# Performance work log

Measured on AMD Instinct MI355X. Metric: run time of the kernel, lower is better.

## Reference

```python
import jax, jax.numpy as jnp
import numpy as np

D, N, K, H, F, L, T, V = 2048, 16, 8, 128, 6144, 2, 2048, 32000
EPS = 1e-6
THETA = 1000000.0

def rms_norm(x, scale, eps=EPS):
    x32 = x.astype(jnp.float32)
    y = x32 * jax.lax.rsqrt(jnp.mean(x32 * x32, axis=-1, keepdims=True) + eps)
    return (y * scale).astype(x.dtype)

def apply_rope(x, pos, dim, theta):
    # x: [T, n, H]; rotate_half style RoPE on first `dim` dims (dim == H here)
    half = dim // 2
    inv_freq = 1.0 / (theta ** (jnp.arange(half, dtype=jnp.float32) / half))
    freqs = pos.astype(jnp.float32)[:, None] * inv_freq  # [T, half]
    cos = jnp.cos(freqs)[:, None, :]
    sin = jnp.sin(freqs)[:, None, :]
    x1, x2 = x[..., :half], x[..., half:]
    return jnp.concatenate([x1 * cos - x2 * sin, x2 * cos + x1 * sin], axis=-1).astype(x.dtype)

def qmatmul(x, w, s):
    # fp8 e4m3 dequant matmul: quantize kernel, upcast, scale per output channel
    wq = w.astype(jnp.float8_e4m3fn).astype(jnp.float32)
    return (x @ wq) * s

def setup_inputs() -> dict:
    key = jax.random.key(0)
    ks = jax.random.split(key, 20)
    w = lambda k, sh, sc=0.02: (jax.random.normal(k, sh, jnp.float32) * sc)
    return {
        'input_ids': jax.random.randint(ks[0], (T,), 0, V, jnp.int32),
        'positions': jnp.arange(T, dtype=jnp.int32),
        'embed': w(ks[1], (V, D), 1.0),
        'ln1': jax.random.uniform(ks[2], (L, D), jnp.float32),
        'q_w': w(ks[3], (L, D, N, H)),
        'q_norm': jax.random.uniform(ks[4], (L, H), jnp.float32),
        'k_w': w(ks[5], (L, D, K, H)),
        'k_norm': jax.random.uniform(ks[6], (L, H), jnp.float32),
        'v_w': w(ks[7], (L, D, K, H)),
        'o_w': w(ks[8], (L, N, H, D)),
        'ln2': jax.random.uniform(ks[9], (L, D), jnp.float32),
        'gate_w': w(ks[10], (L, D, F), 0.1),
        'gate_scale': jax.random.uniform(ks[11], (L, F), jnp.float32, 0.01, 0.05),
        'up_w': w(ks[12], (L, D, F), 0.1),
        'up_scale': jax.random.uniform(ks[13], (L, F), jnp.float32, 0.01, 0.05),
        'down_w': w(ks[14], (L, F, D), 0.1),
        'down_scale': jax.random.uniform(ks[15], (L, D), jnp.float32, 0.01, 0.05),
        'final_norm': jax.random.uniform(ks[16], (D,), jnp.float32),
        'lm_head': w(ks[17], (D, V), 0.02),
    }

def reference(input_ids, positions, embed, ln1, q_w, q_norm, k_w, k_norm, v_w, o_w,
              ln2, gate_w, gate_scale, up_w, up_scale, down_w, down_scale,
              final_norm, lm_head):
    h = embed[input_ids]                                   # [T, D]
    t = h.shape[0]
    sm_scale = 1.0 / np.sqrt(H)
    causal = jnp.tril(jnp.ones((t, t), dtype=bool))
    G = N // K  # GQA group size

    def layer(h, p):
        l1, qw, qn, kw, kn, vw, ow, l2, gw, gs, uw, us, dw, ds = p
        x = rms_norm(h, l1)
        q = rms_norm(jnp.einsum('td,dnh->tnh', x, qw), qn)
        q = apply_rope(q, positions, H, THETA)
        k = rms_norm(jnp.einsum('td,dkh->tkh', x, kw), kn)
        k = apply_rope(k, positions, H, THETA)
        v = jnp.einsum('td,dkh->tkh', x, vw)
        qg = q.reshape(t, K, G, H)
        scores = jnp.einsum('tkgh,skh->kgts', qg, k) * sm_scale
        scores = jnp.where(causal[None, None], scores, -1e30)
        attn = jax.nn.softmax(scores, axis=-1)
        o = jnp.einsum('kgts,skh->tkgh', attn, v).reshape(t, N, H)
        h = h + jnp.einsum('tnh,nhd->td', o, ow)
        x2 = rms_norm(h, l2)
        fuse = jax.nn.silu(qmatmul(x2, gw, gs)) * qmatmul(x2, uw, us)
        h = h + qmatmul(fuse, dw, ds)
        return h, None

    h, _ = jax.lax.scan(layer, h, (ln1, q_w, q_norm, k_w, k_norm, v_w, o_w,
                                   ln2, gate_w, gate_scale, up_w, up_scale,
                                   down_w, down_scale))
    h = rms_norm(h, final_norm)
    return h @ lm_head                                      # [T, V] logits
```

## Files before the change

### kernel.cpp

```cpp
#include <hip/hip_runtime.h>

#define TT 2048
#define DD 2048
#define NHEAD 16
#define KHEAD 8
#define HDIM 128
#define FF 6144
#define LLAYERS 2
#define VV 32000

typedef __attribute__((ext_vector_type(8))) __bf16 bf16x8;
typedef __attribute__((ext_vector_type(4))) float f32x4;

__device__ __forceinline__ unsigned short f2bf(float x) {
  unsigned u = __float_as_uint(x);
  return (unsigned short)((u + 0x7FFFu + ((u >> 16) & 1u)) >> 16);
}

__device__ __forceinline__ float fp8_rt(float x) {
  float ax = fabsf(x);
  if (ax < 0.015625f) return rintf(x * 512.0f) * (1.0f / 512.0f);
  unsigned u = __float_as_uint(x);
  unsigned r = (u + 0x7FFFFu + ((u >> 20) & 1u)) & 0xFFF00000u;
  float y = __uint_as_float(r);
  if (fabsf(y) > 448.0f) y = copysignf(448.0f, x);
  return y;
}

__device__ __forceinline__ void gload16(const void* g, void* l) {
  __builtin_amdgcn_global_load_lds((__attribute__((address_space(1))) void*)g,
                                   (__attribute__((address_space(3))) void*)l,
                                   16, 0, 0);
}

__global__ void k_embed(const int* __restrict__ ids, const float* __restrict__ embed,
                        float* __restrict__ h) {
  int t = blockIdx.x;
  const float4* src = (const float4*)(embed + (size_t)ids[t] * DD);
  float4* dst = (float4*)(h + (size_t)t * DD);
  for (int i = threadIdx.x; i < DD / 4; i += 256) dst[i] = src[i];
}

__global__ void k_rmsnorm(const float* __restrict__ h, const float* __restrict__ g,
                          unsigned short* __restrict__ out) {
  int t = blockIdx.x;
  const float4* row = (const float4*)(h + (size_t)t * DD);
  float4 a = row[threadIdx.x], b = row[threadIdx.x + 256];
  float ss = a.x * a.x + a.y * a.y + a.z * a.z + a.w * a.w +
             b.x * b.x + b.y * b.y + b.z * b.z + b.w * b.w;
#pragma unroll
  for (int m = 32; m >= 1; m >>= 1) ss += __shfl_xor(ss, m);
  __shared__ float sred[4];
  int wid = threadIdx.x >> 6;
  if ((threadIdx.x & 63) == 0) sred[wid] = ss;
  __syncthreads();
  float tot = sred[0] + sred[1] + sred[2] + sred[3];
  float rn = 1.0f / sqrtf(tot * (1.0f / 2048.0f) + 1e-6f);
  const float4* gg = (const float4*)g;
  float4 g0 = gg[threadIdx.x], g1 = gg[threadIdx.x + 256];
  unsigned short* o0 = out + (size_t)t * DD + threadIdx.x * 4;
  unsigned short* o1 = o0 + 1024;
  *(ushort4*)o0 = make_ushort4(f2bf(a.x * rn * g0.x), f2bf(a.y * rn * g0.y),
                               f2bf(a.z * rn * g0.z), f2bf(a.w * rn * g0.w));
  *(ushort4*)o1 = make_ushort4(f2bf(b.x * rn * g1.x), f2bf(b.y * rn * g1.y),
                               f2bf(b.z * rn * g1.z), f2bf(b.w * rn * g1.w));
}

template <bool QUANT>
__global__ void k_wconv(const float* __restrict__ W, unsigned short* __restrict__ Wt,
                        int Kd, int Nd) {
  __shared__ float tile[64][65];
  int k0 = blockIdx.y * 64, n0 = blockIdx.x * 64;
  int t = threadIdx.x;
#pragma unroll
  for (int i = 0; i < 4; ++i) {
    int row = (t >> 4) + i * 16, c4 = (t & 15) * 4;
    float4 v = *(const float4*)&W[(size_t)(k0 + row) * Nd + n0 + c4];
    tile[row][c4] = v.x; tile[row][c4 + 1] = v.y;
    tile[row][c4 + 2] = v.z; tile[row][c4 + 3] = v.w;
  }
  __syncthreads();
#pragma unroll
  for (int i = 0; i < 2; ++i) {
    int n = (t >> 3) + i * 32, kc = (t & 7) * 8;
    unsigned short r[8];
#pragma unroll
    for (int j = 0; j < 8; ++j) {
      float x = tile[kc + j][n];
      if (QUANT) x = fp8_rt(x);
      r[j] = f2bf(x);
    }
    unsigned short* o = &Wt[(size_t)(n0 + n) * Kd + k0 + kc];
    *(ushort4*)o = make_ushort4(r[0], r[1], r[2], r[3]);
    *(ushort4*)(o + 4) = make_ushort4(r[4], r[5], r[6], r[7]);
  }
}

template <int EPI>
__global__ __launch_bounds__(256, 2) void k_gemm(
    const unsigned short* __restrict__ A, const unsigned short* __restrict__ Bt,
    int M, int N, int K, float* __restrict__ Cf, const float* __restrict__ scaleN) {
  __shared__ unsigned short Al[128 * 64];
  __shared__ unsigned short Bl[128 * 64];
  const int tid = threadIdx.x;
  const int lane = tid & 63, wid = tid >> 6;
  const int wm = wid >> 1, wn = wid & 1;
  const int l16 = lane & 15, lg = lane >> 4;
  const size_t m0 = (size_t)blockIdx.x * 128, n0 = (size_t)blockIdx.y * 128;
  f32x4 acc[4][4] = {};
  for (int k0 = 0; k0 < K; k0 += 64) {
    __syncthreads();
#pragma unroll
    for (int it = 0; it < 4; ++it) {
      int chunk = it * 256 + tid;
      int row = chunk >> 3, c8 = chunk & 7;
      const unsigned short* ga = A + (m0 + row) * (size_t)K + k0 + c8 * 8;
      const unsigned short* gb = Bt + (n0 + row) * (size_t)K + k0 + c8 * 8;
      int base = (it * 256 + wid * 64) * 8;
      gload16((const void*)ga, (void*)&Al[base]);
      gload16((const void*)gb, (void*)&Bl[base]);
    }
    __syncthreads();
#pragma unroll
    for (int kk = 0; kk < 2; ++kk) {
      bf16x8 af[4], bfr[4];
      const int kb = kk * 32 + lg * 8;
#pragma unroll
      for (int i = 0; i < 4; ++i)
        af[i] = *(const bf16x8*)&Al[(wm * 64 + i * 16 + l16) * 64 + kb];
#pragma unroll
      for (int i = 0; i < 4; ++i)
        bfr[i] = *(const bf16x8*)&Bl[(wn * 64 + i * 16 + l16) * 64 + kb];
#pragma unroll
      for (int mi = 0; mi < 4; ++mi)
#pragma unroll
        for (int ni = 0; ni < 4; ++ni)
          acc[mi][ni] = __builtin_amdgcn_mfma_f32_16x16x32_bf16(af[mi], bfr[ni],
                                                                acc[mi][ni], 0, 0, 0);
    }
  }
#pragma unroll
  for (int mi = 0; mi < 4; ++mi)
#pragma unroll
    for (int r = 0; r < 4; ++r) {
      size_t row = m0 + wm * 64 + mi * 16 + 4 * lg + r;
#pragma unroll
      for (int ni = 0; ni < 4; ++ni) {
        size_t col = n0 + wn * 64 + ni * 16 + l16;
        float v = acc[mi][ni][r];
        size_t idx = row * (size_t)N + col;
        if constexpr (EPI == 0) Cf[idx] = v;
        else if constexpr (EPI == 1) Cf[idx] += v;
        else Cf[idx] += v * scaleN[col];
      }
    }
}

template <int PT, bool VM, class STG>
__device__ __forceinline__ void gphase(const char* smem, int BUF, int aRd, int bRd,
                                       bf16x8 (&af)[4][2], bf16x8 (&bfr)[2][2][2],
                                       f32x4 (&acc)[8][4], STG&& stage, bool vmzero) {
  constexpr int MH = (PT >= 2) ? 1 : 0;
  constexpr int NH = (PT == 1 || PT == 2) ? 1 : 0;
  if constexpr (PT == 0 || PT == 2) {
#pragma unroll
    for (int m = 0; m < 4; ++m) {
      int abase = BUF + aRd + MH * 8192 + m * 2048;
      af[m][0] = *(const bf16x8*)(smem + abase);
      af[m][1] = *(const bf16x8*)(smem + (abase ^ 64));
    }
  }
  if constexpr (PT <= 1) {
#pragma unroll
    for (int n = 0; n < 2; ++n) {
      int bbase = BUF + bRd + NH * 4096 + n * 2048;
      bfr[NH][n][0] = *(const bf16x8*)(smem + bbase);
      bfr[NH][n][1] = *(const bf16x8*)(smem + (bbase ^ 64));
    }
  }
  stage();
  if (VM) {
    if (vmzero) asm volatile("s_waitcnt vmcnt(0)" ::: "memory");
    else        asm volatile("s_waitcnt vmcnt(4)" ::: "memory");
  }
  __builtin_amdgcn_sched_barrier(0);
  __builtin_amdgcn_s_barrier();
  if constexpr (PT != 3) {
    asm volatile("s_waitcnt lgkmcnt(0)" ::: "memory");
    __builtin_amdgcn_sched_barrier(0);
  }
  __builtin_amdgcn_s_setprio(1);
#pragma unroll
  for (int kk = 0; kk < 2; ++kk)
#pragma unroll
    for (int m = 0; m < 4; ++m)
#pragma unroll
      for (int n = 0; n < 2; ++n)
        acc[MH * 4 + m][NH * 2 + n] = __builtin_amdgcn_mfma_f32_16x16x32_bf16(
            af[m][kk], bfr[NH][n][kk], acc[MH * 4 + m][NH * 2 + n], 0, 0, 0);
  __builtin_amdgcn_s_setprio(0);
  __builtin_amdgcn_sched_barrier(0);
}

template <int EPI>
__global__ __launch_bounds__(512, 2) void k_gemm256(
    const unsigned short* __restrict__ A, const unsigned short* __restrict__ Bt,
    int N, int Kstride, int Kloop, int S, void* __restrict__ Cv) {
  extern __shared__ __align__(16) char smem[];
  const int tid = threadIdx.x;
  const int lane = tid & 63, wid = tid >> 6;
  const int wm = wid >> 2, wn = wid & 3;
  const int l16 = lane & 15, lg = lane >> 4;
  const int l8 = lane >> 3, s8 = lane & 7;

  const int nwg = gridDim.x;
  const int q = nwg >> 3, r = nwg & 7;
  const int xcd = blockIdx.x & 7, loc = blockIdx.x >> 3;
  const int wg = (xcd < r ? xcd * (q + 1) : r * (q + 1) + (xcd - r) * q) + loc;
  const int bm = wg & 7;
  const int t_ = wg >> 3;
  const int split = t_ % S, bn = t_ / S;
  const size_t m0 = (size_t)bm * 256, n0 = (size_t)bn * 256;
  const size_t kofs = (size_t)split * Kloop;

  const char* Ag = (const char*)(A + m0 * (size_t)Kstride + kofs);
  const char* Bg = (const char*)(Bt + n0 * (size_t)Kstride + kofs);
  const size_t sKA = (size_t)Kstride * 128;
  const size_t sKB = (size_t)Kstride * 64;
  const size_t aA = (size_t)(wid * 8 + l8) * Kstride * 2 + (size_t)((s8 ^ l8) << 4);
  const size_t aB = (size_t)((wid & 3) * 8 + l8) * Kstride * 2 + (size_t)((s8 ^ l8) << 4);

  auto stgA = [&](int BUF, int p, int kt) {
    gload16(Ag + aA + (size_t)p * sKA + (size_t)kt * 128,
            smem + BUF + p * 8192 + wid * 1024);
  };
  auto stgB = [&](int BUF, int qa, int qb, int kt) {
    int qq = (wid < 4) ? qa : qb;
    gload16(Bg + aB + (size_t)qq * sKB + (size_t)kt * 128,
            smem + BUF + 32768 + qq * 4096 + (wid & 3) * 1024);
  };
  auto stAev = [&](int BUF, int kt) { stgA(BUF, 0, kt); stgA(BUF, 2, kt); };
  auto stAod = [&](int BUF, int kt) { stgA(BUF, 1, kt); stgA(BUF, 3, kt); };
  auto stBev = [&](int BUF, int kt) { stgB(BUF, 0, 2, kt); stgB(BUF, 4, 6, kt); };
  auto stBod = [&](int BUF, int kt) { stgB(BUF, 1, 3, kt); stgB(BUF, 5, 7, kt); };

  const int colx = (lg << 4) ^ ((l16 & 7) << 4);
  const int aRd = (wm * 128 + l16) * 128 + colx;
  const int bRd = 32768 + (wn * 64 + l16) * 128 + colx;

  f32x4 acc[8][4] = {};
  bf16x8 af[4][2];
  bf16x8 bfr[2][2][2];

  stAev(0, 0); stAod(0, 0); stBev(0, 0); stBod(0, 0);
  stBev(65536, 1); stBod(65536, 1);
  asm volatile("s_waitcnt vmcnt(4)" ::: "memory");
  __builtin_amdgcn_s_barrier();

  const int NIT = Kloop >> 7;
#pragma unroll 1
  for (int i = 0; i < NIT; ++i) {
    const int t1 = 2 * i + 1, t2 = 2 * i + 2, t3 = 2 * i + 3;
    const bool more = (i + 1 < NIT);
    gphase<0, false>(smem, 0, aRd, bRd, af, bfr, acc, [&] { stAev(65536, t1); }, false);
    gphase<1, false>(smem, 0, aRd, bRd, af, bfr, acc, [&] { stAod(65536, t1); }, false);
    gphase<2, false>(smem, 0, aRd, bRd, af, bfr, acc, [&] { if (more) stBev(0, t2); }, false);
    gphase<3, true >(smem, 0, aRd, bRd, af, bfr, acc, [&] { if (more) stBod(0, t2); }, !more);
    gphase<0, false>(smem, 65536, aRd, bRd, af, bfr, acc, [&] { if (more) stAev(0, t2); }, false);
    gphase<1, false>(smem, 65536, aRd, bRd, af, bfr, acc, [&] { if (more) stAod(0, t2); }, false);
    gphase<2, false>(smem, 65536, aRd, bRd, af, bfr, acc, [&] { if (more) stBev(65536, t3); }, false);
    gphase<3, true >(smem, 65536, aRd, bRd, af, bfr, acc, [&] { if (more) stBod(65536, t3); }, false);
  }

  char* Cb = (char*)Cv + (EPI == 0 ? (size_t)split * TT * N * 4 : 0);
#pragma unroll
  for (int m = 0; m < 8; ++m)
#pragma unroll
    for (int rr = 0; rr < 4; ++rr) {
      size_t row = m0 + wm * 128 + m * 16 + lg * 4 + rr;
#pragma unroll
      for (int n = 0; n < 4; ++n) {
        size_t col = n0 + wn * 64 + n * 16 + l16;
        float v = acc[m][n][rr];
        size_t idx = row * (size_t)N + col;
        if constexpr (EPI == 0) ((float*)Cb)[idx] = v;
        else ((unsigned short*)Cb)[idx] = f2bf(v);
      }
    }
}

__global__ void k_sred(const float* __restrict__ p, const float* __restrict__ scale,
                       float* __restrict__ h, int S, int n) {
  int total = TT * n / 4;
  for (int i = blockIdx.x * 256 + threadIdx.x; i < total; i += gridDim.x * 256) {
    float4 s = ((const float4*)p)[i];
    for (int ss = 1; ss < S; ++ss) {
      float4 v = ((const float4*)(p + (size_t)ss * TT * n))[i];
      s.x += v.x; s.y += v.y; s.z += v.z; s.w += v.w;
    }
    if (scale) {
      int col = (i * 4) % n;
      s.x *= scale[col]; s.y *= scale[col + 1];
      s.z *= scale[col + 2]; s.w *= scale[col + 3];
    }
    float4 hv = ((float4*)h)[i];
    hv.x += s.x; hv.y += s.y; hv.z += s.z; hv.w += s.w;
    ((float4*)h)[i] = hv;
  }
}

__global__ void k_swiglu(const unsigned short* __restrict__ gu, const float* __restrict__ gs,
                         const float* __restrict__ us, unsigned short* __restrict__ out) {
  size_t idx = (size_t)blockIdx.x * 256 + threadIdx.x;
  int t = idx / 768, f8 = (int)(idx % 768) * 8;
  const unsigned short* gp = gu + (size_t)t * 12288 + f8;
  ushort4 ga = *(const ushort4*)gp, gb = *(const ushort4*)(gp + 4);
  ushort4 ua = *(const ushort4*)(gp + 6144), ub = *(const ushort4*)(gp + 6148);
  unsigned short* op = out + (size_t)t * FF + f8;
  unsigned short res[8];
  unsigned short gv[8] = {ga.x, ga.y, ga.z, ga.w, gb.x, gb.y, gb.z, gb.w};
  unsigned short uv[8] = {ua.x, ua.y, ua.z, ua.w, ub.x, ub.y, ub.z, ub.w};
#pragma unroll
  for (int j = 0; j < 8; ++j) {
    float g = __uint_as_float((unsigned)gv[j] << 16) * gs[f8 + j];
    float u = __uint_as_float((unsigned)uv[j] << 16) * us[f8 + j];
    float f = (g / (1.0f + expf(-g))) * u;
    res[j] = f2bf(f);
  }
  *(ushort4*)op = make_ushort4(res[0], res[1], res[2], res[3]);
  *(ushort4*)(op + 4) = make_ushort4(res[4], res[5], res[6], res[7]);
}

__global__ void k_qk_post(const float* __restrict__ p0, const float* __restrict__ p1,
                          const float* __restrict__ nscale, const int* __restrict__ pos,
                          unsigned short* __restrict__ out, int nheads, int rstride,
                          int coloff, float qscale) {
  int gw = blockIdx.x * 4 + (threadIdx.x >> 6);
  int t = gw / nheads, n = gw % nheads;
  int lane = threadIdx.x & 63;
  size_t base = (size_t)t * rstride + coloff + n * HDIM;
  float x1 = p0[base + lane] + p1[base + lane];
  float x2 = p0[base + lane + 64] + p1[base + lane + 64];
  float ss = x1 * x1 + x2 * x2;
#pragma unroll
  for (int m = 32; m >= 1; m >>= 1) ss += __shfl_xor(ss, m);
  float rn = qscale / sqrtf(ss * (1.0f / 128.0f) + 1e-6f);
  x1 *= rn * nscale[lane];
  x2 *= rn * nscale[lane + 64];
  float p = (float)pos[t];
  float inv = powf(1.0e6f, -(float)lane / 64.0f);
  float fr = p * inv;
  float c = cosf(fr), s = sinf(fr);
  unsigned short* o = out + ((size_t)n * TT + t) * HDIM;
  o[lane] = f2bf(x1 * c - x2 * s);
  o[lane + 64] = f2bf(x2 * c + x1 * s);
}

__global__ void k_vt(const float* __restrict__ p0, const float* __restrict__ p1,
                     unsigned short* __restrict__ vT, int rstride) {
  __shared__ float tile[32][33];
  int t0 = blockIdx.x * 32, h0 = blockIdx.y * 32;
  int tx = threadIdx.x, ty = threadIdx.y;
#pragma unroll
  for (int i = 0; i < 32; i += 8) {
    size_t idx = (size_t)(t0 + ty + i) * rstride + h0 + tx;
    tile[ty + i][tx] = p0[idx] + p1[idx];
  }
  __syncthreads();
  int kvh = h0 >> 7;
  int hh = h0 & 127;
#pragma unroll
  for (int i = 0; i < 32; i += 8) {
    float x = tile[tx][ty + i];
    vT[(size_t)kvh * HDIM * TT + (size_t)(hh + ty + i) * TT + t0 + tx] = f2bf(x);
  }
}

__global__ __launch_bounds__(256, 2) void k_attn(
    const unsigned short* __restrict__ Qb, const unsigned short* __restrict__ Kb,
    const unsigned short* __restrict__ Vt, unsigned short* __restrict__ Ob) {
  __shared__ __align__(16) char kv[2][32768];
  __shared__ __align__(16) char Pl[4][2048];
  const int tid = threadIdx.x;
  const int w = tid >> 6, lane = tid & 63;
  const int l16 = lane & 15, lg = lane >> 4;
  const int head = blockIdx.y, kvh = head >> 1;
  const int r0 = blockIdx.x * 64 + w * 16;

  bf16x8 qf[4];
  const unsigned short* Qrow = Qb + ((size_t)head * TT + r0 + l16) * HDIM;
#pragma unroll
  for (int kc = 0; kc < 4; ++kc) qf[kc] = *(const bf16x8*)&Qrow[kc * 32 + lg * 8];

  const char* Kh = (const char*)(Kb + (size_t)kvh * TT * HDIM);
  const char* Vh = (const char*)(Vt + (size_t)kvh * HDIM * TT);

  auto stage = [&](int buf, int t) {
    const int kt0 = t * 64;
    char* bk = kv[buf];
    char* bv = kv[buf] + 16384;
#pragma unroll
    for (int it = 0; it < 4; ++it) {
      int rowK = it * 16 + w * 4 + (lane >> 4);
      gload16(Kh + (size_t)(kt0 + rowK) * 256 + (((lane & 15) ^ (rowK & 7)) << 4),
              bk + (it * 256 + w * 64) * 16);
      int rowV = it * 32 + w * 8 + (lane >> 3);
      gload16(Vh + (size_t)rowV * (TT * 2) + (size_t)kt0 * 2 +
                  (((lane & 7) ^ (rowV & 7)) << 4),
              bv + (it * 256 + w * 64) * 16);
    }
  };

  f32x4 o[8] = {};
  float m_[4], l_[4];
#pragma unroll
  for (int r = 0; r < 4; ++r) { m_[r] = -1e30f; l_[r] = 0.0f; }
  char* Pw = Pl[w];

  const int nt = blockIdx.x + 1;
  stage(0, 0);
  asm volatile("s_waitcnt vmcnt(0)" ::: "memory");
  __syncthreads();

#pragma unroll 1
  for (int t = 0; t < nt; ++t) {
    const int buf = t & 1;
    const int kt0 = t * 64;
    if (t + 1 < nt) stage(buf ^ 1, t + 1);
    const char* bk = kv[buf];
    const char* bv = kv[buf] + 16384;

    f32x4 sg[4];
#pragma unroll
    for (int g = 0; g < 4; ++g) {
      sg[g] = f32x4{0.f, 0.f, 0.f, 0.f};
#pragma unroll
      for (int kc = 0; kc < 4; ++kc) {
        int row = g * 16 + l16;
        int slot = kc * 4 + lg;
        bf16x8 kf = *(const bf16x8*)(bk + row * 256 + ((slot ^ (row & 7)) << 4));
        sg[g] = __builtin_amdgcn_mfma_f32_16x16x32_bf16(qf[kc], kf, sg[g], 0, 0, 0);
      }
    }
    f32x4 mx;
#pragma unroll
    for (int r = 0; r < 4; ++r) {
      int row = r0 + 4 * lg + r;
      float a = sg[0][r]; if (kt0 + l16 > row) a = -1e30f; sg[0][r] = a;
      float b = sg[1][r]; if (kt0 + 16 + l16 > row) b = -1e30f; sg[1][r] = b;
      float c = sg[2][r]; if (kt0 + 32 + l16 > row) c = -1e30f; sg[2][r] = c;
      float d = sg[3][r]; if (kt0 + 48 + l16 > row) d = -1e30f; sg[3][r] = d;
      mx[r] = fmaxf(fmaxf(a, b), fmaxf(c, d));
    }
#pragma unroll
    for (int msk = 8; msk >= 1; msk >>= 1)
#pragma unroll
      for (int r = 0; r < 4; ++r) mx[r] = fmaxf(mx[r], __shfl_xor(mx[r], msk));
    float alpha[4];
#pragma unroll
    for (int r = 0; r < 4; ++r) {
      float mn = fmaxf(m_[r], mx[r]);
      alpha[r] = __expf(m_[r] - mn);
      m_[r] = mn;
    }
    f32x4 rs;
#pragma unroll
    for (int r = 0; r < 4; ++r) {
      float s0 = __expf(sg[0][r] - m_[r]);
      float s1 = __expf(sg[1][r] - m_[r]);
      float s2 = __expf(sg[2][r] - m_[r]);
      float s3 = __expf(sg[3][r] - m_[r]);
      sg[0][r] = s0; sg[1][r] = s1; sg[2][r] = s2; sg[3][r] = s3;
      rs[r] = (s0 + s1) + (s2 + s3);
    }
#pragma unroll
    for (int msk = 8; msk >= 1; msk >>= 1)
#pragma unroll
      for (int r = 0; r < 4; ++r) rs[r] += __shfl_xor(rs[r], msk);
#pragma unroll
    for (int r = 0; r < 4; ++r) l_[r] = l_[r] * alpha[r] + rs[r];
#pragma unroll
    for (int hi = 0; hi < 8; ++hi)
#pragma unroll
      for (int r = 0; r < 4; ++r) o[hi][r] *= alpha[r];

#pragma unroll
    for (int g = 0; g < 4; ++g)
#pragma unroll
      for (int r = 0; r < 4; ++r) {
        int prow = 4 * lg + r;
        int slot = g * 2 + (l16 >> 3);
        *(unsigned short*)(Pw + prow * 128 + ((slot ^ (prow & 7)) << 4) +
                           (l16 & 7) * 2) = f2bf(sg[g][r]);
      }
    bf16x8 pf[2];
#pragma unroll
    for (int half = 0; half < 2; ++half) {
      int slot = half * 4 + lg;
      pf[half] = *(const bf16x8*)(Pw + l16 * 128 + ((slot ^ (l16 & 7)) << 4));
    }
#pragma unroll
    for (int hi = 0; hi < 8; ++hi) {
      int row = hi * 16 + l16;
#pragma unroll
      for (int half = 0; half < 2; ++half) {
        int slot = half * 4 + lg;
        bf16x8 vf = *(const bf16x8*)(bv + row * 128 + ((slot ^ (row & 7)) << 4));
        o[hi] = __builtin_amdgcn_mfma_f32_16x16x32_bf16(pf[half], vf, o[hi], 0, 0, 0);
      }
    }
    asm volatile("s_waitcnt vmcnt(0)" ::: "memory");
    __syncthreads();
  }

#pragma unroll
  for (int r = 0; r < 4; ++r) {
    float inv = 1.0f / l_[r];
    size_t t = r0 + 4 * lg + r;
#pragma unroll
    for (int hi = 0; hi < 8; ++hi)
      Ob[t * DD + head * HDIM + hi * 16 + l16] = f2bf(o[hi][r] * inv);
  }
}

extern "C" void kernel_launch(void* const* d_in, const int* in_sizes, int n_in,
                              void* d_out, int out_size, void* d_ws, size_t ws_size,
                              hipStream_t stream) {
  (void)in_sizes; (void)n_in; (void)out_size; (void)ws_size;
  const int* ids = (const int*)d_in[0];
  const int* pos = (const int*)d_in[1];
  const float* embed = (const float*)d_in[2];
  const float* ln1 = (const float*)d_in[3];
  const float* q_w = (const float*)d_in[4];
  const float* q_norm = (const float*)d_in[5];
  const float* k_w = (const float*)d_in[6];
  const float* k_norm = (const float*)d_in[7];
  const float* v_w = (const float*)d_in[8];
  const float* o_w = (const float*)d_in[9];
  const float* ln2 = (const float*)d_in[10];
  const float* gate_w = (const float*)d_in[11];
  const float* gate_s = (const float*)d_in[12];
  const float* up_w = (const float*)d_in[13];
  const float* up_s = (const float*)d_in[14];
  const float* down_w = (const float*)d_in[15];
  const float* down_s = (const float*)d_in[16];
  const float* fnorm = (const float*)d_in[17];
  const float* lm = (const float*)d_in[18];

  hipFuncSetAttribute((const void*)k_gemm256<0>,
                      hipFuncAttributeMaxDynamicSharedMemorySize, 131072);
  hipFuncSetAttribute((const void*)k_gemm256<1>,
                      hipFuncAttributeMaxDynamicSharedMemorySize, 131072);

  char* p = (char*)d_ws;
  auto alloc = [&](size_t n) { char* r = p; p += (n + 255) & ~(size_t)255; return r; };
  unsigned short* wbuf = (unsigned short*)alloc((size_t)VV * DD * 2);
  float* h = (float*)alloc((size_t)TT * DD * 4);
  unsigned short* xb = (unsigned short*)alloc((size_t)TT * DD * 2);
  float* qkvf = (float*)alloc((size_t)2 * TT * 4096 * 4);
  unsigned short* qb = (unsigned short*)alloc((size_t)NHEAD * TT * HDIM * 2);
  unsigned short* kb = (unsigned short*)alloc((size_t)KHEAD * TT * HDIM * 2);
  unsigned short* vT = (unsigned short*)alloc((size_t)KHEAD * HDIM * TT * 2);
  unsigned short* ob = (unsigned short*)alloc((size_t)TT * DD * 2);
  unsigned short* fuse = (unsigned short*)alloc((size_t)TT * FF * 2);
  unsigned short* gbuf = (unsigned short*)((char*)wbuf + ((size_t)64 << 20));
  float* dpart = (float*)((char*)wbuf + ((size_t)56 << 20));
  float* qpart1 = qkvf + (size_t)TT * 4096;
  const float sm = 0.08838834764831845f;

  k_embed<<<TT, 256, 0, stream>>>(ids, embed, h);
  for (int l = 0; l < LLAYERS; ++l) {
    k_rmsnorm<<<TT, 256, 0, stream>>>(h, ln1 + (size_t)l * DD, xb);
    k_wconv<false><<<dim3(2048 / 64, DD / 64), 256, 0, stream>>>(
        q_w + (size_t)l * DD * 2048, wbuf, DD, 2048);
    k_wconv<false><<<dim3(1024 / 64, DD / 64), 256, 0, stream>>>(
        k_w + (size_t)l * DD * 1024, wbuf + (size_t)2048 * DD, DD, 1024);
    k_wconv<false><<<dim3(1024 / 64, DD / 64), 256, 0, stream>>>(
        v_w + (size_t)l * DD * 1024, wbuf + (size_t)3072 * DD, DD, 1024);
    k_gemm256<0><<<8 * (4096 / 256) * 2, 512, 131072, stream>>>(
        xb, wbuf, 4096, DD, 1024, 2, qkvf);
    k_qk_post<<<TT * NHEAD / 4, 256, 0, stream>>>(
        qkvf, qpart1, q_norm + (size_t)l * HDIM, pos, qb, NHEAD, 4096, 0, sm);
    k_qk_post<<<TT * KHEAD / 4, 256, 0, stream>>>(
        qkvf, qpart1, k_norm + (size_t)l * HDIM, pos, kb, KHEAD, 4096, 2048, 1.0f);
    k_vt<<<dim3(TT / 32, 1024 / 32), dim3(32, 8), 0, stream>>>(
        qkvf + 3072, qpart1 + 3072, vT, 4096);
    k_attn<<<dim3(TT / 64, NHEAD), 256, 0, stream>>>(qb, kb, vT, ob);
    k_wconv<false><<<dim3(DD / 64, 2048 / 64), 256, 0, stream>>>(
        o_w + (size_t)l * 2048 * DD, wbuf, 2048, DD);
    k_gemm<1><<<dim3(TT / 128, DD / 128), 256, 0, stream>>>(
        ob, wbuf, TT, DD, 2048, h, nullptr);
    k_rmsnorm<<<TT, 256, 0, stream>>>(h, ln2 + (size_t)l * DD, xb);
    k_wconv<true><<<dim3(FF / 64, DD / 64), 256, 0, stream>>>(
        gate_w + (size_t)l * DD * FF, wbuf, DD, FF);
    k_wconv<true><<<dim3(FF / 64, DD / 64), 256, 0, stream>>>(
        up_w + (size_t)l * DD * FF, wbuf + (size_t)FF * DD, DD, FF);
    k_gemm256<1><<<8 * (12288 / 256), 512, 131072, stream>>>(
        xb, wbuf, 12288, DD, DD, 1, gbuf);
    k_swiglu<<<TT * 768 / 256, 256, 0, stream>>>(
        gbuf, gate_s + (size_t)l * FF, up_s + (size_t)l * FF, fuse);
    k_wconv<true><<<dim3(DD / 64, FF / 64), 256, 0, stream>>>(
        down_w + (size_t)l * FF * DD, wbuf, FF, DD);
    k_gemm256<0><<<8 * (DD / 256) * 4, 512, 131072, stream>>>(
        fuse, wbuf, DD, FF, 1536, 4, dpart);
    k_sred<<<2048, 256, 0, stream>>>(dpart, down_s + (size_t)l * DD, h, 4, DD);
  }
  k_rmsnorm<<<TT, 256, 0, stream>>>(h, fnorm, xb);
  k_wconv<false><<<dim3(VV / 64, DD / 64), 256, 0, stream>>>(lm, wbuf, DD, VV);
  k_gemm256<0><<<8 * (VV / 256), 512, 131072, stream>>>(
      xb, wbuf, VV, DD, DD, 1, d_out);
}
```

Before: 1.280 ms.

## Fuse SwiGLU into gate/up GEMM epilogue via interleaved weights; widen attention query tile

After: 1.291 ms. About the same (+0.9%).

```diff
diff --git a/kernel.cpp b/kernel.cpp
--- a/kernel.cpp
+++ b/kernel.cpp
@@ -96,6 +96,33 @@
   }
 }
 
+__global__ void k_wconv_glu(const float* __restrict__ W, unsigned short* __restrict__ Wt,
+                            int Kd, int Nd, int off) {
+  __shared__ float tile[64][65];
+  int k0 = blockIdx.y * 64, n0 = blockIdx.x * 64;
+  int t = threadIdx.x;
+#pragma unroll
+  for (int i = 0; i < 4; ++i) {
+    int row = (t >> 4) + i * 16, c4 = (t & 15) * 4;
+    float4 v = *(const float4*)&W[(size_t)(k0 + row) * Nd + n0 + c4];
+    tile[row][c4] = v.x; tile[row][c4 + 1] = v.y;
+    tile[row][c4 + 2] = v.z; tile[row][c4 + 3] = v.w;
+  }
+  __syncthreads();
+#pragma unroll
+  for (int i = 0; i < 2; ++i) {
+    int n = (t >> 3) + i * 32, kc = (t & 7) * 8;
+    unsigned short r[8];
+#pragma unroll
+    for (int j = 0; j < 8; ++j) r[j] = f2bf(fp8_rt(tile[kc + j][n]));
+    int lj = n0 + n;
+    int phys = ((lj >> 4) << 5) + (lj & 15) + off;
+    unsigned short* o = &Wt[(size_t)phys * Kd + k0 + kc];
+    *(ushort4*)o = make_ushort4(r[0], r[1], r[2], r[3]);
+    *(ushort4*)(o + 4) = make_ushort4(r[4], r[5], r[6], r[7]);
+  }
+}
+
 template <int EPI>
 __global__ __launch_bounds__(256, 2) void k_gemm(
     const unsigned short* __restrict__ A, const unsigned short* __restrict__ Bt,
@@ -205,7 +232,8 @@
 template <int EPI>
 __global__ __launch_bounds__(512, 2) void k_gemm256(
     const unsigned short* __restrict__ A, const unsigned short* __restrict__ Bt,
-    int N, int Kstride, int Kloop, int S, void* __restrict__ Cv) {
+    int N, int Kstride, int Kloop, int S, void* __restrict__ Cv,
+    const float* __restrict__ gs, const float* __restrict__ us) {
   extern __shared__ __align__(16) char smem[];
   const int tid = threadIdx.x;
   const int lane = tid & 63, wid = tid >> 6;
@@ -272,21 +300,38 @@
     gphase<3, true >(smem, 65536, aRd, bRd, af, bfr, acc, [&] { if (more) stBod(65536, t3); }, false);
   }
 
-  char* Cb = (char*)Cv + (EPI == 0 ? (size_t)split * TT * N * 4 : 0);
-#pragma unroll
-  for (int m = 0; m < 8; ++m)
-#pragma unroll
-    for (int rr = 0; rr < 4; ++rr) {
-      size_t row = m0 + wm * 128 + m * 16 + lg * 4 + rr;
-#pragma unroll
-      for (int n = 0; n < 4; ++n) {
-        size_t col = n0 + wn * 64 + n * 16 + l16;
-        float v = acc[m][n][rr];
-        size_t idx = row * (size_t)N + col;
-        if constexpr (EPI == 0) ((float*)Cb)[idx] = v;
-        else ((unsigned short*)Cb)[idx] = f2bf(v);
-      }
-    }
+  if constexpr (EPI == 2) {
+    const int q0 = (int)((n0 + (size_t)wn * 64) >> 5);
+    const float gsc0 = gs[q0 * 16 + l16], usc0 = us[q0 * 16 + l16];
+    const float gsc1 = gs[(q0 + 1) * 16 + l16], usc1 = us[(q0 + 1) * 16 + l16];
+    unsigned short* F = (unsigned short*)Cv;
+#pragma unroll
+    for (int m = 0; m < 8; ++m)
+#pragma unroll
+      for (int rr = 0; rr < 4; ++rr) {
+        size_t row = m0 + wm * 128 + m * 16 + lg * 4 + rr;
+        float g0 = acc[m][0][rr] * gsc0, u0 = acc[m][1][rr] * usc0;
+        float g1 = acc[m][2][rr] * gsc1, u1 = acc[m][3][rr] * usc1;
+        F[row * FF + q0 * 16 + l16] = f2bf((g0 / (1.0f + __expf(-g0))) * u0);
+        F[row * FF + (q0 + 1) * 16 + l16] = f2bf((g1 / (1.0f + __expf(-g1))) * u1);
+      }
+  } else {
+    char* Cb = (char*)Cv + (EPI == 0 ? (size_t)split * TT * N * 4 : 0);
+#pragma unroll
+    for (int m = 0; m < 8; ++m)
+#pragma unroll
+      for (int rr = 0; rr < 4; ++rr) {
+        size_t row = m0 + wm * 128 + m * 16 + lg * 4 + rr;
+#pragma unroll
+        for (int n = 0; n < 4; ++n) {
+          size_t col = n0 + wn * 64 + n * 16 + l16;
+          float v = acc[m][n][rr];
+          size_t idx = row * (size_t)N + col;
+          if constexpr (EPI == 0) ((float*)Cb)[idx] = v;
+          else ((unsigned short*)Cb)[idx] = f2bf(v);
+        }
+      }
+  }
 }
 
 __global__ void k_sred(const float* __restrict__ p, const float* __restrict__ scale,
@@ -307,28 +352,6 @@
     hv.x += s.x; hv.y += s.y; hv.z += s.z; hv.w += s.w;
     ((float4*)h)[i] = hv;
   }
-}
-
-__global__ void k_swiglu(const unsigned short* __restrict__ gu, const float* __restrict__ gs,
-                         const float* __restrict__ us, unsigned short* __restrict__ out) {
-  size_t idx = (size_t)blockIdx.x * 256 + threadIdx.x;
-  int t = idx / 768, f8 = (int)(idx % 768) * 8;
-  const unsigned short* gp = gu + (size_t)t * 12288 + f8;
-  ushort4 ga = *(const ushort4*)gp, gb = *(const ushort4*)(gp + 4);
-  ushort4 ua = *(const ushort4*)(gp + 6144), ub = *(const ushort4*)(gp + 6148);
-  unsigned short* op = out + (size_t)t * FF + f8;
-  unsigned short res[8];
-  unsigned short gv[8] = {ga.x, ga.y, ga.z, ga.w, gb.x, gb.y, gb.z, gb.w};
-  unsigned short uv[8] = {ua.x, ua.y, ua.z, ua.w, ub.x, ub.y, ub.z, ub.w};
-#pragma unroll
-  for (int j = 0; j < 8; ++j) {
-    float g = __uint_as_float((unsigned)gv[j] << 16) * gs[f8 + j];
-    float u = __uint_as_float((unsigned)uv[j] << 16) * us[f8 + j];
-    float f = (g / (1.0f + expf(-g))) * u;
-    res[j] = f2bf(f);
-  }
-  *(ushort4*)op = make_ushort4(res[0], res[1], res[2], res[3]);
-  *(ushort4*)(op + 4) = make_ushort4(res[4], res[5], res[6], res[7]);
 }
 
 __global__ void k_qk_post(const float* __restrict__ p0, const float* __restrict__ p1,
@@ -385,12 +408,15 @@
   const int w = tid >> 6, lane = tid & 63;
   const int l16 = lane & 15, lg = lane >> 4;
   const int head = blockIdx.y, kvh = head >> 1;
-  const int r0 = blockIdx.x * 64 + w * 16;
-
-  bf16x8 qf[4];
-  const unsigned short* Qrow = Qb + ((size_t)head * TT + r0 + l16) * HDIM;
-#pragma unroll
-  for (int kc = 0; kc < 4; ++kc) qf[kc] = *(const bf16x8*)&Qrow[kc * 32 + lg * 8];
+  const int r0 = blockIdx.x * 128 + w * 32;
+
+  bf16x8 qf[2][4];
+#pragma unroll
+  for (int qg = 0; qg < 2; ++qg) {
+    const unsigned short* Qrow = Qb + ((size_t)head * TT + r0 + qg * 16 + l16) * HDIM;
+#pragma unroll
+    for (int kc = 0; kc < 4; ++kc) qf[qg][kc] = *(const bf16x8*)&Qrow[kc * 32 + lg * 8];
+  }
 
   const char* Kh = (const char*)(Kb + (size_t)kvh * TT * HDIM);
   const char* Vh = (const char*)(Vt + (size_t)kvh * HDIM * TT);
@@ -411,13 +437,15 @@
     }
   };
 
-  f32x4 o[8] = {};
-  float m_[4], l_[4];
-#pragma unroll
-  for (int r = 0; r < 4; ++r) { m_[r] = -1e30f; l_[r] = 0.0f; }
+  f32x4 o[2][8] = {};
+  float m_[2][4], l_[2][4];
+#pragma unroll
+  for (int qg = 0; qg < 2; ++qg)
+#pragma unroll
+    for (int r = 0; r < 4; ++r) { m_[qg][r] = -1e30f; l_[qg][r] = 0.0f; }
   char* Pw = Pl[w];
 
-  const int nt = blockIdx.x + 1;
+  const int nt = 2 * (blockIdx.x + 1);
   stage(0, 0);
   asm volatile("s_waitcnt vmcnt(0)" ::: "memory");
   __syncthreads();
@@ -430,83 +458,86 @@
     const char* bk = kv[buf];
     const char* bv = kv[buf] + 16384;
 
-    f32x4 sg[4];
-#pragma unroll
-    for (int g = 0; g < 4; ++g) {
-      sg[g] = f32x4{0.f, 0.f, 0.f, 0.f};
-#pragma unroll
-      for (int kc = 0; kc < 4; ++kc) {
-        int row = g * 16 + l16;
-        int slot = kc * 4 + lg;
-        bf16x8 kf = *(const bf16x8*)(bk + row * 256 + ((slot ^ (row & 7)) << 4));
-        sg[g] = __builtin_amdgcn_mfma_f32_16x16x32_bf16(qf[kc], kf, sg[g], 0, 0, 0);
-      }
-    }
-    f32x4 mx;
-#pragma unroll
-    for (int r = 0; r < 4; ++r) {
-      int row = r0 + 4 * lg + r;
-      float a = sg[0][r]; if (kt0 + l16 > row) a = -1e30f; sg[0][r] = a;
-      float b = sg[1][r]; if (kt0 + 16 + l16 > row) b = -1e30f; sg[1][r] = b;
-      float c = sg[2][r]; if (kt0 + 32 + l16 > row) c = -1e30f; sg[2][r] = c;
-      float d = sg[3][r]; if (kt0 + 48 + l16 > row) d = -1e30f; sg[3][r] = d;
-      mx[r] = fmaxf(fmaxf(a, b), fmaxf(c, d));
-    }
-#pragma unroll
-    for (int msk = 8; msk >= 1; msk >>= 1)
-#pragma unroll
-      for (int r = 0; r < 4; ++r) mx[r] = fmaxf(mx[r], __shfl_xor(mx[r], msk));
-    float alpha[4];
-#pragma unroll
-    for (int r = 0; r < 4; ++r) {
-      float mn = fmaxf(m_[r], mx[r]);
-      alpha[r] = __expf(m_[r] - mn);
-      m_[r] = mn;
-    }
-    f32x4 rs;
-#pragma unroll
-    for (int r = 0; r < 4; ++r) {
-      float s0 = __expf(sg[0][r] - m_[r]);
-      float s1 = __expf(sg[1][r] - m_[r]);
-      float s2 = __expf(sg[2][r] - m_[r]);
-      float s3 = __expf(sg[3][r] - m_[r]);
-      sg[0][r] = s0; sg[1][r] = s1; sg[2][r] = s2; sg[3][r] = s3;
-      rs[r] = (s0 + s1) + (s2 + s3);
-    }
-#pragma unroll
-    for (int msk = 8; msk >= 1; msk >>= 1)
-#pragma unroll
-      for (int r = 0; r < 4; ++r) rs[r] += __shfl_xor(rs[r], msk);
-#pragma unroll
-    for (int r = 0; r < 4; ++r) l_[r] = l_[r] * alpha[r] + rs[r];
-#pragma unroll
-    for (int hi = 0; hi < 8; ++hi)
-#pragma unroll
-      for (int r = 0; r < 4; ++r) o[hi][r] *= alpha[r];
-
-#pragma unroll
-    for (int g = 0; g < 4; ++g)
+#pragma unroll
+    for (int qg = 0; qg < 2; ++qg) {
+      f32x4 sg[4];
+#pragma unroll
+      for (int cg = 0; cg < 4; ++cg) {
+        sg[cg] = f32x4{0.f, 0.f, 0.f, 0.f};
+#pragma unroll
+        for (int kc = 0; kc < 4; ++kc) {
+          int row = cg * 16 + l16;
+          int slot = kc * 4 + lg;
+          bf16x8 kf = *(const bf16x8*)(bk + row * 256 + ((slot ^ (row & 7)) << 4));
+          sg[cg] = __builtin_amdgcn_mfma_f32_16x16x32_bf16(qf[qg][kc], kf, sg[cg], 0, 0, 0);
+        }
+      }
+      f32x4 mx;
 #pragma unroll
       for (int r = 0; r < 4; ++r) {
-        int prow = 4 * lg + r;
-        int slot = g * 2 + (l16 >> 3);
-        *(unsigned short*)(Pw + prow * 128 + ((slot ^ (prow & 7)) << 4) +
-                           (l16 & 7) * 2) = f2bf(sg[g][r]);
-      }
-    bf16x8 pf[2];
-#pragma unroll
-    for (int half = 0; half < 2; ++half) {
-      int slot = half * 4 + lg;
-      pf[half] = *(const bf16x8*)(Pw + l16 * 128 + ((slot ^ (l16 & 7)) << 4));
-    }
-#pragma unroll
-    for (int hi = 0; hi < 8; ++hi) {
-      int row = hi * 16 + l16;
+        int row = r0 + qg * 16 + 4 * lg + r;
+        float a = sg[0][r]; if (kt0 + l16 > row) a = -1e30f; sg[0][r] = a;
+        float b = sg[1][r]; if (kt0 + 16 + l16 > row) b = -1e30f; sg[1][r] = b;
+        float c = sg[2][r]; if (kt0 + 32 + l16 > row) c = -1e30f; sg[2][r] = c;
+        float d = sg[3][r]; if (kt0 + 48 + l16 > row) d = -1e30f; sg[3][r] = d;
+        mx[r] = fmaxf(fmaxf(a, b), fmaxf(c, d));
+      }
+#pragma unroll
+      for (int msk = 8; msk >= 1; msk >>= 1)
+#pragma unroll
+        for (int r = 0; r < 4; ++r) mx[r] = fmaxf(mx[r], __shfl_xor(mx[r], msk));
+      float alpha[4];
+#pragma unroll
+      for (int r = 0; r < 4; ++r) {
+        float mn = fmaxf(m_[qg][r], mx[r]);
+        alpha[r] = __expf(m_[qg][r] - mn);
+        m_[qg][r] = mn;
+      }
+      f32x4 rs;
+#pragma unroll
+      for (int r = 0; r < 4; ++r) {
+        float s0 = __expf(sg[0][r] - m_[qg][r]);
+        float s1 = __expf(sg[1][r] - m_[qg][r]);
+        float s2 = __expf(sg[2][r] - m_[qg][r]);
+        float s3 = __expf(sg[3][r] - m_[qg][r]);
+        sg[0][r] = s0; sg[1][r] = s1; sg[2][r] = s2; sg[3][r] = s3;
+        rs[r] = (s0 + s1) + (s2 + s3);
+      }
+#pragma unroll
+      for (int msk = 8; msk >= 1; msk >>= 1)
+#pragma unroll
+        for (int r = 0; r < 4; ++r) rs[r] += __shfl_xor(rs[r], msk);
+#pragma unroll
+      for (int r = 0; r < 4; ++r) l_[qg][r] = l_[qg][r] * alpha[r] + rs[r];
+#pragma unroll
+      for (int hi = 0; hi < 8; ++hi)
+#pragma unroll
+        for (int r = 0; r < 4; ++r) o[qg][hi][r] *= alpha[r];
+
+#pragma unroll
+      for (int cg = 0; cg < 4; ++cg)
+#pragma unroll
+        for (int r = 0; r < 4; ++r) {
+          int prow = 4 * lg + r;
+          int slot = cg * 2 + (l16 >> 3);
+          *(unsigned short*)(Pw + prow * 128 + ((slot ^ (prow & 7)) << 4) +
+                             (l16 & 7) * 2) = f2bf(sg[cg][r]);
+        }
+      bf16x8 pf[2];
 #pragma unroll
       for (int half = 0; half < 2; ++half) {
         int slot = half * 4 + lg;
-        bf16x8 vf = *(const bf16x8*)(bv + row * 128 + ((slot ^ (row & 7)) << 4));
-        o[hi] = __builtin_amdgcn_mfma_f32_16x16x32_bf16(pf[half], vf, o[hi], 0, 0, 0);
+        pf[half] = *(const bf16x8*)(Pw + l16 * 128 + ((slot ^ (l16 & 7)) << 4));
+      }
+#pragma unroll
+      for (int hi = 0; hi < 8; ++hi) {
+        int row = hi * 16 + l16;
+#pragma unroll
+        for (int half = 0; half < 2; ++half) {
+          int slot = half * 4 + lg;
+          bf16x8 vf = *(const bf16x8*)(bv + row * 128 + ((slot ^ (row & 7)) << 4));
+          o[qg][hi] = __builtin_amdgcn_mfma_f32_16x16x32_bf16(pf[half], vf, o[qg][hi], 0, 0, 0);
+        }
       }
     }
     asm volatile("s_waitcnt vmcnt(0)" ::: "memory");
@@ -514,13 +545,15 @@
   }
 
 #pragma unroll
-  for (int r = 0; r < 4; ++r) {
-    float inv = 1.0f / l_[r];
-    size_t t = r0 + 4 * lg + r;
-#pragma unroll
-    for (int hi = 0; hi < 8; ++hi)
-      Ob[t * DD + head * HDIM + hi * 16 + l16] = f2bf(o[hi][r] * inv);
-  }
+  for (int qg = 0; qg < 2; ++qg)
+#pragma unroll
+    for (int r = 0; r < 4; ++r) {
+      float inv = 1.0f / l_[qg][r];
+      size_t t = r0 + qg * 16 + 4 * lg + r;
+#pragma unroll
+      for (int hi = 0; hi < 8; ++hi)
+        Ob[t * DD + head * HDIM + hi * 16 + l16] = f2bf(o[qg][hi][r] * inv);
+    }
 }
 
 extern "C" void kernel_launch(void* const* d_in, const int* in_sizes, int n_in,
@@ -551,6 +584,8 @@
                       hipFuncAttributeMaxDynamicSharedMemorySize, 131072);
   hipFuncSetAttribute((const void*)k_gemm256<1>,
                       hipFuncAttributeMaxDynamicSharedMemorySize, 131072);
+  hipFuncSetAttribute((const void*)k_gemm256<2>,
+                      hipFuncAttributeMaxDynamicSharedMemorySize, 131072);
 
   char* p = (char*)d_ws;
   auto alloc = [&](size_t n) { char* r = p; p += (n + 255) & ~(size_t)255; return r; };
@@ -563,7 +598,6 @@
   unsigned short* vT = (unsigned short*)alloc((size_t)KHEAD * HDIM * TT * 2);
   unsigned short* ob = (unsigned short*)alloc((size_t)TT * DD * 2);
   unsigned short* fuse = (unsigned short*)alloc((size_t)TT * FF * 2);
-  unsigned short* gbuf = (unsigned short*)((char*)wbuf + ((size_t)64 << 20));
   float* dpart = (float*)((char*)wbuf + ((size_t)56 << 20));
   float* qpart1 = qkvf + (size_t)TT * 4096;
   const float sm = 0.08838834764831845f;
@@ -578,35 +612,34 @@
     k_wconv<false><<<dim3(1024 / 64, DD / 64), 256, 0, stream>>>(
         v_w + (size_t)l * DD * 1024, wbuf + (size_t)3072 * DD, DD, 1024);
     k_gemm256<0><<<8 * (4096 / 256) * 2, 512, 131072, stream>>>(
-        xb, wbuf, 4096, DD, 1024, 2, qkvf);
+        xb, wbuf, 4096, DD, 1024, 2, qkvf, nullptr, nullptr);
     k_qk_post<<<TT * NHEAD / 4, 256, 0, stream>>>(
         qkvf, qpart1, q_norm + (size_t)l * HDIM, pos, qb, NHEAD, 4096, 0, sm);
     k_qk_post<<<TT * KHEAD / 4, 256, 0, stream>>>(
         qkvf, qpart1, k_norm + (size_t)l * HDIM, pos, kb, KHEAD, 4096, 2048, 1.0f);
     k_vt<<<dim3(TT / 32, 1024 / 32), dim3(32, 8), 0, stream>>>(
         qkvf + 3072, qpart1 + 3072, vT, 4096);
-    k_attn<<<dim3(TT / 64, NHEAD), 256, 0, stream>>>(qb, kb, vT, ob);
+    k_attn<<<dim3(TT / 128, NHEAD), 256, 0, stream>>>(qb, kb, vT, ob);
     k_wconv<false><<<dim3(DD / 64, 2048 / 64), 256, 0, stream>>>(
         o_w + (size_t)l * 2048 * DD, wbuf, 2048, DD);
     k_gemm<1><<<dim3(TT / 128, DD / 128), 256, 0, stream>>>(
         ob, wbuf, TT, DD, 2048, h, nullptr);
     k_rmsnorm<<<TT, 256, 0, stream>>>(h, ln2 + (size_t)l * DD, xb);
-    k_wconv<true><<<dim3(FF / 64, DD / 64), 256, 0, stream>>>(
-        gate_w + (size_t)l * DD * FF, wbuf, DD, FF);
-    k_wconv<true><<<dim3(FF / 64, DD / 64), 256, 0, stream>>>(
-        up_w + (size_t)l * DD * FF, wbuf + (size_t)FF * DD, DD, FF);
-    k_gemm256<1><<<8 * (12288 / 256), 512, 131072, stream>>>(
-        xb, wbuf, 12288, DD, DD, 1, gbuf);
-    k_swiglu<<<TT * 768 / 256, 256, 0, stream>>>(
-        gbuf, gate_s + (size_t)l * FF, up_s + (size_t)l * FF, fuse);
+    k_wconv_glu<<<dim3(FF / 64, DD / 64), 256, 0, stream>>>(
+        gate_w + (size_t)l * DD * FF, wbuf, DD, FF, 0);
+    k_wconv_glu<<<dim3(FF / 64, DD / 64), 256, 0, stream>>>(
+        up_w + (size_t)l * DD * FF, wbuf, DD, FF, 16);
+    k_gemm256<2><<<8 * (12288 / 256), 512, 131072, stream>>>(
+        xb, wbuf, 12288, DD, DD, 1, fuse, gate_s + (size_t)l * FF,
+        up_s + (size_t)l * FF);
     k_wconv<true><<<dim3(DD / 64, FF / 64), 256, 0, stream>>>(
         down_w + (size_t)l * FF * DD, wbuf, FF, DD);
     k_gemm256<0><<<8 * (DD / 256) * 4, 512, 131072, stream>>>(
-        fuse, wbuf, DD, FF, 1536, 4, dpart);
+        fuse, wbuf, DD, FF, 1536, 4, dpart, nullptr, nullptr);
     k_sred<<<2048, 256, 0, stream>>>(dpart, down_s + (size_t)l * DD, h, 4, DD);
   }
   k_rmsnorm<<<TT, 256, 0, stream>>>(h, fnorm, xb);
   k_wconv<false><<<dim3(VV / 64, DD / 64), 256, 0, stream>>>(lm, wbuf, DD, VV);
   k_gemm256<0><<<8 * (VV / 256), 512, 131072, stream>>>(
-      xb, wbuf, VV, DD, DD, 1, d_out);
-}
+      xb, wbuf, VV, DD, DD, 1, d_out, nullptr, nullptr);
+}
```
